# Kernel optimization log

Hardware: AMD Instinct MI355X
Metric: run time of the kernel (lower is better)

The kernel has to match this reference:

```python
import jax, jax.numpy as jnp
import numpy as np

B = 524288
D_IN = 128
H = 16          # hard-coded by amax slicing in MLSTMCell
D_OUT = 4


def _quant(x, amax):
    # torch quant_tensor: clamp(round(x * 127/amax), -127, 127) -> int8 (kept as
    # integer-valued float32 here; exact since |v| <= 127)
    if amax.ndim > 1:
        amax = jnp.squeeze(amax, 1)
    return jnp.clip(jnp.round(x * (127.0 / amax)), -127.0, 127.0)


def _dequant(x, amax, double=False):
    max_range = 127.0 ** 2 if double else 127.0
    scale = max_range / amax
    if scale.ndim > 1:
        scale = jnp.squeeze(scale, 1)
    return x / scale


def setup_inputs() -> dict:
    key = jax.random.key(0)
    ks = jax.random.split(key, 13)
    # weights are stored pre-quantized int8 (integer-valued); torch casts them
    # to int32 before matmul, so integer-valued float32 is bit-exact in fp32
    intw = lambda k, shp: jax.random.randint(k, shp, -127, 128).astype(jnp.float32)
    x = jax.random.normal(ks[0], (B, D_IN), dtype=jnp.float32)
    h = jax.random.normal(ks[1], (B, H), dtype=jnp.float32) * 0.1
    c = jax.random.normal(ks[2], (B, H), dtype=jnp.float32) * 0.1
    w1 = intw(ks[3], (H, D_IN))          # net.0.weight
    w_ih = intw(ks[4], (4 * H, H))       # lstm.weight_ih
    w_hh = intw(ks[5], (4 * H, H))       # lstm.weight_hh
    w_out = intw(ks[6], (D_OUT, H))      # output_layer.weight
    u = lambda k, shp, lo, hi: jax.random.uniform(k, shp, minval=lo, maxval=hi, dtype=jnp.float32)
    amax_in0 = u(ks[7], (), 1.0, 4.0)            # net.0._input_quantizer._amax (per-tensor)
    amax_w0 = u(ks[8], (H, 1), 32.0, 127.0)      # net.0._weight_quantizer._amax (per-channel)
    amax_lstm_in = u(ks[9], (), 1.0, 4.0)        # lstm._input_quantizer._amax
    amax_w_lstm = u(ks[10], (4 * H, 1), 32.0, 127.0)  # lstm._weight_quantizer._amax
    amax_out_in = u(ks[11], (), 1.0, 4.0)        # output_layer._input_quantizer._amax
    amax_w_out = u(ks[12], (D_OUT, 1), 32.0, 127.0)   # output_layer._weight_quantizer._amax
    return dict(x=x, h=h, c=c, w1=w1, w_ih=w_ih, w_hh=w_hh, w_out=w_out,
                amax_in0=amax_in0, amax_w0=amax_w0, amax_lstm_in=amax_lstm_in,
                amax_w_lstm=amax_w_lstm, amax_out_in=amax_out_in, amax_w_out=amax_w_out)


def reference(x, h, c, w1, w_ih, w_hh, w_out, amax_in0, amax_w0,
              amax_lstm_in, amax_w_lstm, amax_out_in, amax_w_out):
    # --- fc_1: quantize input, int matmul, relu, requantize for lstm ---
    xq = _quant(x, amax_in0)                     # [B, D_IN] int8-valued
    a = xq @ w1.T                                # [B, H] int32-valued (exact in fp32)
    a = jnp.maximum(a, 0.0)                      # relu
    a = _quant(_dequant(a, amax_in0 * amax_w0, double=True), amax_lstm_in)  # [B, H]
    # --- quantize hidden state (hc arrives as float) ---
    hq = _quant(h, amax_lstm_in)
    cq = _quant(c, amax_lstm_in)
    # --- MLSTMCell ---
    amax = amax_lstm_in * amax_w_lstm            # [4H, 1]
    gates = a @ w_ih.T + hq @ w_hh.T             # [B, 4H] int32-valued
    gates = _dequant(gates, amax, double=True)
    i, f, g, o = jnp.split(gates, 4, axis=1)
    gates = jnp.concatenate([jax.nn.sigmoid(i), jax.nn.sigmoid(f),
                             jnp.tanh(g), jax.nn.sigmoid(o)], axis=1)
    gq = _quant(gates, amax)                     # [B, 4H] int8-valued
    i, f, g, o = jnp.split(gq, 4, axis=1)
    cy = (_dequant(f * cq, amax[16:32] * 3.4764, double=True)
          + _dequant(i * g, amax[:16] * amax[32:48], double=True))
    od = _dequant(o, amax[48:], double=False)
    hy = od * jnp.tanh(cy)
    # --- output layer ---
    xo = _quant(hy, amax_out_in) @ w_out.T       # [B, D_OUT]
    xo = _dequant(xo, amax_out_in * amax_w_out, double=True)
    return xo, hy, cy
```

## Files before the change

kernel.cpp:

```cpp
#include <hip/hip_runtime.h>
#include <math.h>
#include <limits.h>


#define OFF_QS    0
#define OFF_SFC1  4
#define OFF_SG    20
#define OFF_QG    84
#define OFF_SCF   148
#define OFF_SCIG  164
#define OFF_SOD   180
#define OFF_SXO   196
#define OFF_VBG   200
#define OFF_TI    216
#define OFF_TF    280
#define OFF_TO    344
#define OFF_TG    408
#define OFF_IGT   536
#define OFF_ODT   1064
#define OFF_W1P   1192
#define OFF_WIHP  1704
#define OFF_WHHP  1960
#define OFF_WOUTP 2216

__device__ __forceinline__ float qclip(float v) {
    return fminf(fmaxf(v, -127.0f), 127.0f);
}

__device__ __forceinline__ int sdot4(int a, int b, int c) {
#if __has_builtin(__builtin_amdgcn_sdot4)
    return __builtin_amdgcn_sdot4(a, b, c, false);
#else
    c += ((a << 24) >> 24) * ((b << 24) >> 24);
    c += ((a << 16) >> 24) * ((b << 16) >> 24);
    c += ((a << 8)  >> 24) * ((b << 8)  >> 24);
    c += (a >> 24) * (b >> 24);
    return c;
#endif
}

__device__ __forceinline__ int pack4i(int a, int b, int c, int d) {
    return (a & 255) | ((b & 255) << 8) | ((c & 255) << 16) | (d << 24);
}

__device__ __forceinline__ int pack4f(const float* p) {
    return pack4i((int)p[0], (int)p[1], (int)p[2], (int)p[3]);
}

typedef __attribute__((address_space(1))) const void g_void;
typedef __attribute__((address_space(3))) void l_void;

__device__ __forceinline__ void stage16(const float* g, float* l) {
    __builtin_amdgcn_global_load_lds((g_void*)g, (l_void*)l, 16, 0, 0);
}

#define WAIT_VM0()   { asm volatile("s_waitcnt vmcnt(0)" ::: "memory"); __builtin_amdgcn_sched_barrier(0); }
#define WAIT_VM4()   { asm volatile("s_waitcnt vmcnt(4)" ::: "memory"); __builtin_amdgcn_sched_barrier(0); }
#define WAIT_LGKM0() { asm volatile("s_waitcnt lgkmcnt(0)" ::: "memory"); __builtin_amdgcn_sched_barrier(0); }

__device__ __forceinline__ int qeval_sig(int gi, float s, float q) {
    float v = (float)gi / s;
    float a = 1.0f / (1.0f + expf(-v));
    return (int)qclip(rintf(a * q));
}
__device__ __forceinline__ int qeval_tanh(int gi, float s, float q) {
    float v = (float)gi / s;
    float a = tanhf(v);
    return (int)qclip(rintf(a * q));
}

#define GLIM 1048576

__device__ int search_thr_sig(float s, float q, int target) {
    if (qeval_sig(GLIM, s, q) < target) return INT_MAX;
    int lo = -GLIM, hi = GLIM;
    while (hi - lo > 1) {
        int mid = lo + ((hi - lo) >> 1);
        if (qeval_sig(mid, s, q) >= target) hi = mid; else lo = mid;
    }
    return hi;
}
__device__ int search_thr_tanh(float s, float q, int target) {
    if (qeval_tanh(GLIM, s, q) < target) return INT_MAX;
    int lo = -GLIM, hi = GLIM;
    while (hi - lo > 1) {
        int mid = lo + ((hi - lo) >> 1);
        if (qeval_tanh(mid, s, q) >= target) hi = mid; else lo = mid;
    }
    return hi;
}

__global__ void __launch_bounds__(1024) setup_all(
    const float* __restrict__ w1, const float* __restrict__ w_ih,
    const float* __restrict__ w_hh, const float* __restrict__ w_out,
    const float* __restrict__ a_in0, const float* __restrict__ a_w0,
    const float* __restrict__ a_lstm, const float* __restrict__ a_wl,
    const float* __restrict__ a_out, const float* __restrict__ a_wo,
    float* __restrict__ wsf)
{
    const int t = threadIdx.x;
    int* wsi = (int*)wsf;
    const float amax_in0 = a_in0[0], amax_lstm = a_lstm[0], amax_out = a_out[0];

    if (t == 0) {
        wsf[OFF_QS + 0] = 127.0f / amax_in0;
        wsf[OFF_QS + 1] = 127.0f / amax_lstm;
        wsf[OFF_QS + 2] = 127.0f / amax_out;
    }
    if (t < 16) wsf[OFF_SFC1 + t] = 16129.0f / (amax_in0 * a_w0[t]);
    if (t < 64) {
        float am = amax_lstm * a_wl[t];
        wsf[OFF_SG + t] = 16129.0f / am;
        wsf[OFF_QG + t] = 127.0f / am;
    }
    if (t < 16) {
        float amf = amax_lstm * a_wl[16 + t];
        wsf[OFF_SCF + t] = 16129.0f / (amf * 3.4764f);
        float amo = amax_lstm * a_wl[48 + t];
        wsf[OFF_SOD + t] = 127.0f / amo;
        float ami = amax_lstm * a_wl[t];
        float amg = amax_lstm * a_wl[32 + t];
        wsf[OFF_SCIG + t] = 16129.0f / (ami * amg);
        float s = 16129.0f / amg, q = 127.0f / amg;
        wsi[OFF_VBG + t] = qeval_tanh(-GLIM, s, q);
    }
    if (t < 4) wsf[OFF_SXO + t] = 16129.0f / (amax_out * a_wo[t]);

    if (t < 512) wsi[OFF_W1P + t]  = pack4f(w1 + 4 * t);
    if (t < 256) { wsi[OFF_WIHP + t] = pack4f(w_ih + 4 * t);
                   wsi[OFF_WHHP + t] = pack4f(w_hh + 4 * t); }
    if (t < 16)  wsi[OFF_WOUTP + t] = pack4f(w_out + 4 * t);

    if (t < 64) {
        int m = t >> 2, k = t & 3;
        float am = amax_lstm * a_wl[m];
        wsi[OFF_TI + t] = search_thr_sig(16129.0f / am, 127.0f / am, k + 1);
    } else if (t < 128) {
        int u = t - 64, m = u >> 2, k = u & 3;
        float am = amax_lstm * a_wl[16 + m];
        wsi[OFF_TF + u] = search_thr_sig(16129.0f / am, 127.0f / am, k + 1);
    } else if (t < 192) {
        int u = t - 128, m = u >> 2, k = u & 3;
        float am = amax_lstm * a_wl[48 + m];
        wsi[OFF_TO + u] = search_thr_sig(16129.0f / am, 127.0f / am, k + 1);
    } else if (t < 320) {
        int u = t - 192, m = u >> 3, k = u & 7;
        float am = amax_lstm * a_wl[32 + m];
        float s = 16129.0f / am, q = 127.0f / am;
        int vb = qeval_tanh(-GLIM, s, q);
        wsi[OFF_TG + u] = search_thr_tanh(s, q, vb + 1 + k);
    } else if (t < 848) {
        int u = t - 320, m = u / 33, p = u % 33;
        float ami = amax_lstm * a_wl[m];
        float amg = amax_lstm * a_wl[32 + m];
        float scig = 16129.0f / (ami * amg);
        wsf[OFF_IGT + u] = (float)(p - 16) / scig;
    } else if (t < 928) {
        int u = t - 848, m = u / 5, oq = u % 5;
        float amo = amax_lstm * a_wl[48 + m];
        float sod = 127.0f / amo;
        wsf[OFF_ODT + m * 8 + oq] = (float)oq / sod;
    }
}

__global__ void __launch_bounds__(256) mlpq_kernel(
    const float* __restrict__ x, const float* __restrict__ h, const float* __restrict__ c,
    const float* __restrict__ wsf,
    float* __restrict__ out_xo, float* __restrict__ out_hy, float* __restrict__ out_cy,
    int nrows)
{
    __shared__ float s_tab[656];
    __shared__ __align__(1024) float s_stage[4][2048];

    for (int i = threadIdx.x; i < 656; i += 256) s_tab[i] = wsf[OFF_IGT + i];
    __syncthreads();
    const float* s_igt = s_tab;
    const float* s_odt = s_tab + 528;

    const int tid = threadIdx.x;
    const int wv  = tid >> 6;
    const int rl  = tid & 63;
    const int wrow0 = blockIdx.x * 256 + wv * 64;
    const int r = wrow0 + rl;

    const int sw = (rl >> 1) & 3;
    const int qs_stage = (rl & 3) ^ ((rl >> 3) & 3);
    const int rstage = wrow0 + (rl >> 2);

    float* bufE = &s_stage[wv][0];
    float* bufO = &s_stage[wv][1024];

    const int* __restrict__ wsi = (const int*)wsf;
    const float qs_in   = wsf[OFF_QS + 0];
    const float qs_lstm = wsf[OFF_QS + 1];
    const float qs_out  = wsf[OFF_QS + 2];

    const float* gph = h + (size_t)rstage * 16 + qs_stage * 4;
    const float* gpc = c + (size_t)rstage * 16 + qs_stage * 4;
    const float* gpx = x + (size_t)rstage * 128 + qs_stage * 4;

    stage16(gph + 0 * 256, bufO + 0 * 256);
    stage16(gph + 1 * 256, bufO + 1 * 256);
    stage16(gph + 2 * 256, bufO + 2 * 256);
    stage16(gph + 3 * 256, bufO + 3 * 256);
    stage16(gpx + 0 * 2048, bufE + 0 * 256);
    stage16(gpx + 1 * 2048, bufE + 1 * 256);
    stage16(gpx + 2 * 2048, bufE + 2 * 256);
    stage16(gpx + 3 * 2048, bufE + 3 * 256);

    WAIT_VM4();
    float4 hv[4];
    {
        const float4* b4 = reinterpret_cast<const float4*>(bufO);
#pragma unroll
        for (int q = 0; q < 4; ++q) hv[q] = b4[rl * 4 + (q ^ sw)];
    }
    WAIT_LGKM0();
    {
        const float* g = gpx + 1 * 16;
        stage16(g + 0 * 2048, bufO + 0 * 256);
        stage16(g + 1 * 2048, bufO + 1 * 256);
        stage16(g + 2 * 2048, bufO + 2 * 256);
        stage16(g + 3 * 2048, bufO + 3 * 256);
    }
    int hql[4];
#pragma unroll
    for (int q = 0; q < 4; ++q) {
        float4 v = hv[q];
        hql[q] = pack4i((int)qclip(rintf(v.x * qs_lstm)),
                        (int)qclip(rintf(v.y * qs_lstm)),
                        (int)qclip(rintf(v.z * qs_lstm)),
                        (int)qclip(rintf(v.w * qs_lstm)));
    }

    int acc[16];
#pragma unroll
    for (int j = 0; j < 16; ++j) acc[j] = 0;

#pragma unroll
    for (int kc = 0; kc < 8; ++kc) {
        WAIT_VM4();
        float* bk = (kc & 1) ? bufO : bufE;
        const float4* b4 = reinterpret_cast<const float4*>(bk);
        float4 xv[4];
#pragma unroll
        for (int q = 0; q < 4; ++q) xv[q] = b4[rl * 4 + (q ^ sw)];
        WAIT_LGKM0();
        if (kc <= 5) {
            const float* g = gpx + (kc + 2) * 16;
            stage16(g + 0 * 2048, bk + 0 * 256);
            stage16(g + 1 * 2048, bk + 1 * 256);
            stage16(g + 2 * 2048, bk + 2 * 256);
            stage16(g + 3 * 2048, bk + 3 * 256);
        } else if (kc == 6) {
            stage16(gpc + 0 * 256, bk + 0 * 256);
            stage16(gpc + 1 * 256, bk + 1 * 256);
            stage16(gpc + 2 * 256, bk + 2 * 256);
            stage16(gpc + 3 * 256, bk + 3 * 256);
        }
#pragma unroll
        for (int q = 0; q < 4; ++q) {
            float4 v = xv[q];
            int w = pack4i((int)qclip(rintf(v.x * qs_in)),
                           (int)qclip(rintf(v.y * qs_in)),
                           (int)qclip(rintf(v.z * qs_in)),
                           (int)qclip(rintf(v.w * qs_in)));
#pragma unroll
            for (int j = 0; j < 16; ++j)
                acc[j] = sdot4(w, wsi[OFF_W1P + j * 32 + kc * 4 + q], acc[j]);
        }
    }

    int aql[4];
#pragma unroll
    for (int jg = 0; jg < 4; ++jg) {
        int q[4];
#pragma unroll
        for (int u = 0; u < 4; ++u) {
            int j = jg * 4 + u;
            int ai = acc[j] > 0 ? acc[j] : 0;
            float dq = (float)ai / wsf[OFF_SFC1 + j];
            q[u] = (int)qclip(rintf(dq * qs_lstm));
        }
        aql[jg] = pack4i(q[0], q[1], q[2], q[3]);
    }

    WAIT_VM0();

    const float4* c4 = reinterpret_cast<const float4*>(bufE);
    float hyv[16], cyv[16];
    int xqi[16];

#pragma unroll
    for (int mg = 0; mg < 4; ++mg) {
        float4 cv = c4[rl * 4 + (mg ^ sw)];
        float cvals[4] = {cv.x, cv.y, cv.z, cv.w};
#pragma unroll
        for (int t = 0; t < 4; ++t) {
            const int m = mg * 4 + t;
            int gi = 0, gf = 0, gg = 0, go = 0;
#pragma unroll
            for (int p = 0; p < 4; ++p) {
                int ap = aql[p], hp = hql[p];
                gi = sdot4(ap, wsi[OFF_WIHP + (m)      * 4 + p], gi);
                gi = sdot4(hp, wsi[OFF_WHHP + (m)      * 4 + p], gi);
                gf = sdot4(ap, wsi[OFF_WIHP + (m + 16) * 4 + p], gf);
                gf = sdot4(hp, wsi[OFF_WHHP + (m + 16) * 4 + p], gf);
                gg = sdot4(ap, wsi[OFF_WIHP + (m + 32) * 4 + p], gg);
                gg = sdot4(hp, wsi[OFF_WHHP + (m + 32) * 4 + p], gg);
                go = sdot4(ap, wsi[OFF_WIHP + (m + 48) * 4 + p], go);
                go = sdot4(hp, wsi[OFF_WHHP + (m + 48) * 4 + p], go);
            }
            int iq = (gi >= wsi[OFF_TI + m * 4 + 0]) + (gi >= wsi[OFF_TI + m * 4 + 1])
                   + (gi >= wsi[OFF_TI + m * 4 + 2]) + (gi >= wsi[OFF_TI + m * 4 + 3]);
            int fq = (gf >= wsi[OFF_TF + m * 4 + 0]) + (gf >= wsi[OFF_TF + m * 4 + 1])
                   + (gf >= wsi[OFF_TF + m * 4 + 2]) + (gf >= wsi[OFF_TF + m * 4 + 3]);
            int oq = (go >= wsi[OFF_TO + m * 4 + 0]) + (go >= wsi[OFF_TO + m * 4 + 1])
                   + (go >= wsi[OFF_TO + m * 4 + 2]) + (go >= wsi[OFF_TO + m * 4 + 3]);
            int gq = wsi[OFF_VBG + m]
                   + (gg >= wsi[OFF_TG + m * 8 + 0]) + (gg >= wsi[OFF_TG + m * 8 + 1])
                   + (gg >= wsi[OFF_TG + m * 8 + 2]) + (gg >= wsi[OFF_TG + m * 8 + 3])
                   + (gg >= wsi[OFF_TG + m * 8 + 4]) + (gg >= wsi[OFF_TG + m * 8 + 5])
                   + (gg >= wsi[OFF_TG + m * 8 + 6]) + (gg >= wsi[OFF_TG + m * 8 + 7]);

            int cqv = (int)qclip(rintf(cvals[t] * qs_lstm));

            float cy = (float)(fq * cqv) / wsf[OFF_SCF + m]
                     + s_igt[m * 33 + (iq * gq + 16)];
            float od = s_odt[m * 8 + oq];
            float hy = od * tanhf(cy);

            hyv[m] = hy;
            cyv[m] = cy;
            xqi[m] = (int)qclip(rintf(hy * qs_out));
        }
    }

    int xql[4];
#pragma unroll
    for (int p = 0; p < 4; ++p)
        xql[p] = pack4i(xqi[p * 4], xqi[p * 4 + 1], xqi[p * 4 + 2], xqi[p * 4 + 3]);

    float4 xov;
    {
        int s0 = 0, s1 = 0, s2 = 0, s3 = 0;
#pragma unroll
        for (int p = 0; p < 4; ++p) {
            s0 = sdot4(xql[p], wsi[OFF_WOUTP + 0 * 4 + p], s0);
            s1 = sdot4(xql[p], wsi[OFF_WOUTP + 1 * 4 + p], s1);
            s2 = sdot4(xql[p], wsi[OFF_WOUTP + 2 * 4 + p], s2);
            s3 = sdot4(xql[p], wsi[OFF_WOUTP + 3 * 4 + p], s3);
        }
        xov.x = (float)s0 / wsf[OFF_SXO + 0];
        xov.y = (float)s1 / wsf[OFF_SXO + 1];
        xov.z = (float)s2 / wsf[OFF_SXO + 2];
        xov.w = (float)s3 / wsf[OFF_SXO + 3];
    }

    float4* __restrict__ hyrow = reinterpret_cast<float4*>(out_hy) + (size_t)r * 4;
    float4* __restrict__ cyrow = reinterpret_cast<float4*>(out_cy) + (size_t)r * 4;
#pragma unroll
    for (int mg = 0; mg < 4; ++mg)
        hyrow[mg] = make_float4(hyv[mg * 4], hyv[mg * 4 + 1], hyv[mg * 4 + 2], hyv[mg * 4 + 3]);
#pragma unroll
    for (int mg = 0; mg < 4; ++mg)
        cyrow[mg] = make_float4(cyv[mg * 4], cyv[mg * 4 + 1], cyv[mg * 4 + 2], cyv[mg * 4 + 3]);
    reinterpret_cast<float4*>(out_xo)[r] = xov;
}

extern "C" void kernel_launch(void* const* d_in, const int* in_sizes, int n_in,
                              void* d_out, int out_size, void* d_ws, size_t ws_size,
                              hipStream_t stream) {
    const float* x      = (const float*)d_in[0];
    const float* h      = (const float*)d_in[1];
    const float* c      = (const float*)d_in[2];
    const float* w1     = (const float*)d_in[3];
    const float* w_ih   = (const float*)d_in[4];
    const float* w_hh   = (const float*)d_in[5];
    const float* w_out  = (const float*)d_in[6];
    const float* a_in0  = (const float*)d_in[7];
    const float* a_w0   = (const float*)d_in[8];
    const float* a_lstm = (const float*)d_in[9];
    const float* a_wl   = (const float*)d_in[10];
    const float* a_out  = (const float*)d_in[11];
    const float* a_wo   = (const float*)d_in[12];

    const int B = in_sizes[0] / 128;
    float* out    = (float*)d_out;
    float* out_xo = out;
    float* out_hy = out + (size_t)B * 4;
    float* out_cy = out + (size_t)B * 20;
    float* wsf    = (float*)d_ws;

    hipLaunchKernelGGL(setup_all, dim3(1), dim3(1024), 0, stream,
                       w1, w_ih, w_hh, w_out, a_in0, a_w0, a_lstm, a_wl, a_out, a_wo, wsf);

    dim3 block(256);
    dim3 grid((B + 255) / 256);
    hipLaunchKernelGGL(mlpq_kernel, grid, block, 0, stream,
                       x, h, c, wsf, out_xo, out_hy, out_cy, B);
}
```

Baseline: 109.0 us.

## Single-buffer LDS staging and raise occupancy with launch bounds 256,8

```diff
diff --git a/kernel.cpp b/kernel.cpp
--- a/kernel.cpp
+++ b/kernel.cpp
@@ -55,7 +55,6 @@
 }
 
 #define WAIT_VM0()   { asm volatile("s_waitcnt vmcnt(0)" ::: "memory"); __builtin_amdgcn_sched_barrier(0); }
-#define WAIT_VM4()   { asm volatile("s_waitcnt vmcnt(4)" ::: "memory"); __builtin_amdgcn_sched_barrier(0); }
 #define WAIT_LGKM0() { asm volatile("s_waitcnt lgkmcnt(0)" ::: "memory"); __builtin_amdgcn_sched_barrier(0); }
 
 __device__ __forceinline__ int qeval_sig(int gi, float s, float q) {
@@ -126,7 +125,10 @@
     }
     if (t < 4) wsf[OFF_SXO + t] = 16129.0f / (amax_out * a_wo[t]);
 
-    if (t < 512) wsi[OFF_W1P + t]  = pack4f(w1 + 4 * t);
+    if (t < 512) {
+        int kc = t >> 6, q = (t >> 4) & 3, j = t & 15;
+        wsi[OFF_W1P + t] = pack4f(w1 + j * 128 + kc * 16 + q * 4);
+    }
     if (t < 256) { wsi[OFF_WIHP + t] = pack4f(w_ih + 4 * t);
                    wsi[OFF_WHHP + t] = pack4f(w_hh + 4 * t); }
     if (t < 16)  wsi[OFF_WOUTP + t] = pack4f(w_out + 4 * t);
@@ -163,14 +165,14 @@
     }
 }
 
-__global__ void __launch_bounds__(256) mlpq_kernel(
+__global__ void __launch_bounds__(256, 8) mlpq_kernel(
     const float* __restrict__ x, const float* __restrict__ h, const float* __restrict__ c,
     const float* __restrict__ wsf,
     float* __restrict__ out_xo, float* __restrict__ out_hy, float* __restrict__ out_cy,
     int nrows)
 {
     __shared__ float s_tab[656];
-    __shared__ __align__(1024) float s_stage[4][2048];
+    __shared__ __align__(1024) float s_stage[4][1024];
 
     for (int i = threadIdx.x; i < 656; i += 256) s_tab[i] = wsf[OFF_IGT + i];
     __syncthreads();
@@ -187,8 +189,8 @@
     const int qs_stage = (rl & 3) ^ ((rl >> 3) & 3);
     const int rstage = wrow0 + (rl >> 2);
 
-    float* bufE = &s_stage[wv][0];
-    float* bufO = &s_stage[wv][1024];
+    float* buf = &s_stage[wv][0];
+    const float4* buf4 = reinterpret_cast<const float4*>(buf);
 
     const int* __restrict__ wsi = (const int*)wsf;
     const float qs_in   = wsf[OFF_QS + 0];
@@ -199,30 +201,19 @@
     const float* gpc = c + (size_t)rstage * 16 + qs_stage * 4;
     const float* gpx = x + (size_t)rstage * 128 + qs_stage * 4;
 
-    stage16(gph + 0 * 256, bufO + 0 * 256);
-    stage16(gph + 1 * 256, bufO + 1 * 256);
-    stage16(gph + 2 * 256, bufO + 2 * 256);
-    stage16(gph + 3 * 256, bufO + 3 * 256);
-    stage16(gpx + 0 * 2048, bufE + 0 * 256);
-    stage16(gpx + 1 * 2048, bufE + 1 * 256);
-    stage16(gpx + 2 * 2048, bufE + 2 * 256);
-    stage16(gpx + 3 * 2048, bufE + 3 * 256);
-
-    WAIT_VM4();
+    stage16(gph + 0 * 256, buf + 0 * 256);
+    stage16(gph + 1 * 256, buf + 1 * 256);
+    stage16(gph + 2 * 256, buf + 2 * 256);
+    stage16(gph + 3 * 256, buf + 3 * 256);
+    WAIT_VM0();
     float4 hv[4];
-    {
-        const float4* b4 = reinterpret_cast<const float4*>(bufO);
-#pragma unroll
-        for (int q = 0; q < 4; ++q) hv[q] = b4[rl * 4 + (q ^ sw)];
-    }
+#pragma unroll
+    for (int q = 0; q < 4; ++q) hv[q] = buf4[rl * 4 + (q ^ sw)];
     WAIT_LGKM0();
-    {
-        const float* g = gpx + 1 * 16;
-        stage16(g + 0 * 2048, bufO + 0 * 256);
-        stage16(g + 1 * 2048, bufO + 1 * 256);
-        stage16(g + 2 * 2048, bufO + 2 * 256);
-        stage16(g + 3 * 2048, bufO + 3 * 256);
-    }
+    stage16(gpx + 0 * 2048, buf + 0 * 256);
+    stage16(gpx + 1 * 2048, buf + 1 * 256);
+    stage16(gpx + 2 * 2048, buf + 2 * 256);
+    stage16(gpx + 3 * 2048, buf + 3 * 256);
     int hql[4];
 #pragma unroll
     for (int q = 0; q < 4; ++q) {
@@ -237,27 +228,18 @@
 #pragma unroll
     for (int j = 0; j < 16; ++j) acc[j] = 0;
 
-#pragma unroll
-    for (int kc = 0; kc < 8; ++kc) {
-        WAIT_VM4();
-        float* bk = (kc & 1) ? bufO : bufE;
-        const float4* b4 = reinterpret_cast<const float4*>(bk);
+#pragma unroll 1
+    for (int kc = 0; kc < 7; ++kc) {
+        WAIT_VM0();
         float4 xv[4];
 #pragma unroll
-        for (int q = 0; q < 4; ++q) xv[q] = b4[rl * 4 + (q ^ sw)];
+        for (int q = 0; q < 4; ++q) xv[q] = buf4[rl * 4 + (q ^ sw)];
         WAIT_LGKM0();
-        if (kc <= 5) {
-            const float* g = gpx + (kc + 2) * 16;
-            stage16(g + 0 * 2048, bk + 0 * 256);
-            stage16(g + 1 * 2048, bk + 1 * 256);
-            stage16(g + 2 * 2048, bk + 2 * 256);
-            stage16(g + 3 * 2048, bk + 3 * 256);
-        } else if (kc == 6) {
-            stage16(gpc + 0 * 256, bk + 0 * 256);
-            stage16(gpc + 1 * 256, bk + 1 * 256);
-            stage16(gpc + 2 * 256, bk + 2 * 256);
-            stage16(gpc + 3 * 256, bk + 3 * 256);
-        }
+        const float* g = gpx + (kc + 1) * 16;
+        stage16(g + 0 * 2048, buf + 0 * 256);
+        stage16(g + 1 * 2048, buf + 1 * 256);
+        stage16(g + 2 * 2048, buf + 2 * 256);
+        stage16(g + 3 * 2048, buf + 3 * 256);
 #pragma unroll
         for (int q = 0; q < 4; ++q) {
             float4 v = xv[q];
@@ -265,9 +247,33 @@
                            (int)qclip(rintf(v.y * qs_in)),
                            (int)qclip(rintf(v.z * qs_in)),
                            (int)qclip(rintf(v.w * qs_in)));
+            const int* wrow = wsi + OFF_W1P + kc * 64 + q * 16;
 #pragma unroll
             for (int j = 0; j < 16; ++j)
-                acc[j] = sdot4(w, wsi[OFF_W1P + j * 32 + kc * 4 + q], acc[j]);
+                acc[j] = sdot4(w, wrow[j], acc[j]);
+        }
+    }
+    {
+        WAIT_VM0();
+        float4 xv[4];
+#pragma unroll
+        for (int q = 0; q < 4; ++q) xv[q] = buf4[rl * 4 + (q ^ sw)];
+        WAIT_LGKM0();
+        stage16(gpc + 0 * 256, buf + 0 * 256);
+        stage16(gpc + 1 * 256, buf + 1 * 256);
+        stage16(gpc + 2 * 256, buf + 2 * 256);
+        stage16(gpc + 3 * 256, buf + 3 * 256);
+#pragma unroll
+        for (int q = 0; q < 4; ++q) {
+            float4 v = xv[q];
+            int w = pack4i((int)qclip(rintf(v.x * qs_in)),
+                           (int)qclip(rintf(v.y * qs_in)),
+                           (int)qclip(rintf(v.z * qs_in)),
+                           (int)qclip(rintf(v.w * qs_in)));
+            const int* wrow = wsi + OFF_W1P + 7 * 64 + q * 16;
+#pragma unroll
+            for (int j = 0; j < 16; ++j)
+                acc[j] = sdot4(w, wrow[j], acc[j]);
         }
     }
 
@@ -287,14 +293,16 @@
 
     WAIT_VM0();
 
-    const float4* c4 = reinterpret_cast<const float4*>(bufE);
-    float hyv[16], cyv[16];
-    int xqi[16];
+    float4* __restrict__ hyrow = reinterpret_cast<float4*>(out_hy) + (size_t)r * 4;
+    float4* __restrict__ cyrow = reinterpret_cast<float4*>(out_cy) + (size_t)r * 4;
+    int xql[4];
 
 #pragma unroll
     for (int mg = 0; mg < 4; ++mg) {
-        float4 cv = c4[rl * 4 + (mg ^ sw)];
+        float4 cv = buf4[rl * 4 + (mg ^ sw)];
         float cvals[4] = {cv.x, cv.y, cv.z, cv.w};
+        float hy4[4], cy4[4];
+        int xq4[4];
 #pragma unroll
         for (int t = 0; t < 4; ++t) {
             const int m = mg * 4 + t;
@@ -330,16 +338,14 @@
             float od = s_odt[m * 8 + oq];
             float hy = od * tanhf(cy);
 
-            hyv[m] = hy;
-            cyv[m] = cy;
-            xqi[m] = (int)qclip(rintf(hy * qs_out));
-        }
-    }
-
-    int xql[4];
-#pragma unroll
-    for (int p = 0; p < 4; ++p)
-        xql[p] = pack4i(xqi[p * 4], xqi[p * 4 + 1], xqi[p * 4 + 2], xqi[p * 4 + 3]);
+            hy4[t] = hy;
+            cy4[t] = cy;
+            xq4[t] = (int)qclip(rintf(hy * qs_out));
+        }
+        hyrow[mg] = make_float4(hy4[0], hy4[1], hy4[2], hy4[3]);
+        cyrow[mg] = make_float4(cy4[0], cy4[1], cy4[2], cy4[3]);
+        xql[mg] = pack4i(xq4[0], xq4[1], xq4[2], xq4[3]);
+    }
 
     float4 xov;
     {
@@ -356,15 +362,6 @@
         xov.z = (float)s2 / wsf[OFF_SXO + 2];
         xov.w = (float)s3 / wsf[OFF_SXO + 3];
     }
-
-    float4* __restrict__ hyrow = reinterpret_cast<float4*>(out_hy) + (size_t)r * 4;
-    float4* __restrict__ cyrow = reinterpret_cast<float4*>(out_cy) + (size_t)r * 4;
-#pragma unroll
-    for (int mg = 0; mg < 4; ++mg)
-        hyrow[mg] = make_float4(hyv[mg * 4], hyv[mg * 4 + 1], hyv[mg * 4 + 2], hyv[mg * 4 + 3]);
-#pragma unroll
-    for (int mg = 0; mg < 4; ++mg)
-        cyrow[mg] = make_float4(cyv[mg * 4], cyv[mg * 4 + 1], cyv[mg * 4 + 2], cyv[mg * 4 + 3]);
     reinterpret_cast<float4*>(out_xo)[r] = xov;
 }
 
```

After: 124.0 us. +13.8%, slower.
